# Performance work log

Measured on AMD Instinct MI355X. Metric: run time of the kernel, lower is better.

The kernel has to match this reference:

```python
import jax, jax.numpy as jnp
import numpy as np

E, P, H, V = 512, 640, 512, 1024

def setup_inputs() -> dict:
    key = jax.random.key(0)
    ks = jax.random.split(key, 8)
    s = lambda d: 1.0 / np.sqrt(d)
    return {
        "encoder_output": jax.random.normal(ks[0], (4, 256, E), jnp.float32),
        "prediction_output": jax.random.normal(ks[1], (4, 64, P), jnp.float32),
        "W_enc": jax.random.uniform(ks[2], (E, H), jnp.float32, -s(E), s(E)),
        "b_enc": jax.random.uniform(ks[3], (H,), jnp.float32, -s(E), s(E)),
        "W_pred": jax.random.uniform(ks[4], (P, H), jnp.float32, -s(P), s(P)),
        "b_pred": jax.random.uniform(ks[5], (H,), jnp.float32, -s(P), s(P)),
        "W_out": jax.random.uniform(ks[6], (H, V), jnp.float32, -s(H), s(H)),
        "b_out": jax.random.uniform(ks[7], (V,), jnp.float32, -s(H), s(H)),
    }

def reference(encoder_output, prediction_output, W_enc, b_enc, W_pred, b_pred, W_out, b_out):
    # (B,T,H) and (B,U,H) projections
    enc = jnp.einsum('bte,eh->bth', encoder_output, W_enc) + b_enc
    pred = jnp.einsum('bup,ph->buh', prediction_output, W_pred) + b_pred
    # broadcast add -> (B,T,U,H), ReLU, (dropout is identity in eval), final linear -> (B,T,U,V)
    joint = jax.nn.relu(enc[:, :, None, :] + pred[:, None, :, :])
    return jnp.einsum('btuh,hv->btuv', joint, W_out) + b_out
```

## Files before the change

### kernel.cpp

```cpp
#include <hip/hip_runtime.h>
#include <hip/hip_bf16.h>


typedef __attribute__((ext_vector_type(4))) float f32x4;
typedef __attribute__((ext_vector_type(8))) short bf16x8;

__device__ __forceinline__ short f2bf(float x) {
    return __builtin_bit_cast(short, __float2bfloat16(x));
}

__device__ __forceinline__ int swz(int r, int kByte) {
    return r * 128 + (kByte ^ ((r & 7) << 4));
}

__device__ __forceinline__ int eswz(int r, int vByte) {
    return r * 512 + (vByte ^ ((r & 7) << 4));
}

__global__ void prep_kernel(const float* __restrict__ W_enc,
                            const float* __restrict__ W_pred,
                            const float* __restrict__ W_out,
                            short* __restrict__ WencT,
                            short* __restrict__ WpredT,
                            short* __restrict__ WoutT) {
    const float* in; short* out; int R, C;
    switch (blockIdx.z) {
        case 0:  in = W_enc;  out = WencT;  R = 512; C = 512;  break;
        case 1:  in = W_pred; out = WpredT; R = 640; C = 512;  break;
        default: in = W_out;  out = WoutT;  R = 512; C = 1024; break;
    }
    const int c0 = blockIdx.x * 32, r0 = blockIdx.y * 32;
    if (c0 >= C || r0 >= R) return;

    __shared__ float tile[32][33];
    const int tx = threadIdx.x, ty = threadIdx.y;
    #pragma unroll
    for (int i = 0; i < 32; i += 8) {
        int r = r0 + ty + i, c = c0 + tx;
        if (r < R && c < C) tile[ty + i][tx] = in[(size_t)r * C + c];
    }
    __syncthreads();
    #pragma unroll
    for (int i = 0; i < 32; i += 8) {
        int oc = c0 + ty + i;
        int orr = r0 + tx;
        if (oc < C && orr < R) out[(size_t)oc * R + orr] = f2bf(tile[tx][ty + i]);
    }
}

__global__ __launch_bounds__(256, 2)
void proj_kernel(const float* __restrict__ encIn, const float* __restrict__ predIn,
                 const short* __restrict__ WencT, const short* __restrict__ WpredT,
                 const float* __restrict__ b_enc, const float* __restrict__ b_pred,
                 float* __restrict__ encA, float* __restrict__ predA) {
    const float* A; const short* BT; const float* bias; float* C;
    int M, K;
    if (blockIdx.z == 0) {
        A = encIn;  BT = WencT;  bias = b_enc;  C = encA;  M = 1024; K = 512;
    } else {
        A = predIn; BT = WpredT; bias = b_pred; C = predA; M = 256;  K = 640;
        if ((int)blockIdx.x * 128 >= M) return;
    }
    const int N = 512;

    __shared__ __align__(16) unsigned char lA[128 * 128];
    __shared__ __align__(16) unsigned char lB[128 * 128];

    const int tid = threadIdx.x;
    const int m0 = blockIdx.x * 128;
    const int n0 = blockIdx.y * 128;

    const int rSt = tid >> 3;
    const int kc  = tid & 7;

    const int wave = tid >> 6, lane = tid & 63;
    const int wr = wave >> 1, wc = wave & 1;
    const int rA0 = wr * 64 + (lane & 15);
    const int rB0 = wc * 64 + (lane & 15);
    const int kHi = (lane >> 4) * 16;

    f32x4 acc[4][4];
    #pragma unroll
    for (int i = 0; i < 4; ++i)
        #pragma unroll
        for (int j = 0; j < 4; ++j) acc[i][j] = (f32x4)0.0f;

    for (int k0 = 0; k0 < K; k0 += 64) {
        #pragma unroll
        for (int it = 0; it < 4; ++it) {
            int r = rSt + it * 32;
            const float* ap = A + (size_t)(m0 + r) * K + k0 + kc * 8;
            f32x4 a0 = *(const f32x4*)ap;
            f32x4 a1 = *(const f32x4*)(ap + 4);
            bf16x8 v;
            v[0] = f2bf(a0[0]); v[1] = f2bf(a0[1]); v[2] = f2bf(a0[2]); v[3] = f2bf(a0[3]);
            v[4] = f2bf(a1[0]); v[5] = f2bf(a1[1]); v[6] = f2bf(a1[2]); v[7] = f2bf(a1[3]);
            *(bf16x8*)(lA + swz(r, kc * 16)) = v;
        }
        #pragma unroll
        for (int it = 0; it < 4; ++it) {
            int rn = rSt + it * 32;
            const short* wp = BT + (size_t)(n0 + rn) * K + k0 + kc * 8;
            *(bf16x8*)(lB + swz(rn, kc * 16)) = *(const bf16x8*)wp;
        }
        __syncthreads();
        #pragma unroll
        for (int ks = 0; ks < 2; ++ks) {
            const int kb = ks * 64 + kHi;
            bf16x8 af[4], bf[4];
            #pragma unroll
            for (int i = 0; i < 4; ++i) af[i] = *(const bf16x8*)(lA + swz(rA0 + i * 16, kb));
            #pragma unroll
            for (int j = 0; j < 4; ++j) bf[j] = *(const bf16x8*)(lB + swz(rB0 + j * 16, kb));
            #pragma unroll
            for (int i = 0; i < 4; ++i)
                #pragma unroll
                for (int j = 0; j < 4; ++j)
                    acc[i][j] = __builtin_amdgcn_mfma_f32_16x16x32_bf16(af[i], bf[j], acc[i][j], 0, 0, 0);
        }
        __syncthreads();
    }

    #pragma unroll
    for (int i = 0; i < 4; ++i) {
        #pragma unroll
        for (int j = 0; j < 4; ++j) {
            int col = n0 + wc * 64 + j * 16 + (lane & 15);
            float bo = bias[col];
            #pragma unroll
            for (int rg = 0; rg < 4; ++rg) {
                int row = m0 + wr * 64 + i * 16 + (lane >> 4) * 4 + rg;
                C[(size_t)row * N + col] = acc[i][j][rg] + bo;
            }
        }
    }
}

__global__ __launch_bounds__(256, 2)
void joint_kernel(const float* __restrict__ encA,
                  const float* __restrict__ predA,
                  const short* __restrict__ WoutT,
                  const float* __restrict__ b_out,
                  float* __restrict__ out) {
    __shared__ __align__(16) unsigned char lA[128 * 128];
    __shared__ __align__(16) unsigned char lB[256 * 128];

    const int tid = threadIdx.x;
    const int m0 = blockIdx.x * 128;
    const int n0 = blockIdx.y * 256;
    const int b  = m0 >> 14;
    const int t0 = (m0 >> 6) & 255;

    const int rSt = tid >> 3;
    const int kc  = tid & 7;

    const int wave = tid >> 6, lane = tid & 63;
    const int wr = wave >> 1, wc = wave & 1;
    const int rA0 = wr * 64 + (lane & 15);
    const int rB0 = wc * 128 + (lane & 15);
    const int kHi = (lane >> 4) * 16;

    const float* encB  = encA + (size_t)(b * 256 + t0) * 512;
    const float* predB = predA + (size_t)(b * 64) * 512;

    f32x4 acc[4][8];
    #pragma unroll
    for (int i = 0; i < 4; ++i)
        #pragma unroll
        for (int j = 0; j < 8; ++j) acc[i][j] = (f32x4)0.0f;

    for (int k0 = 0; k0 < 512; k0 += 64) {
        #pragma unroll
        for (int it = 0; it < 4; ++it) {
            int r = rSt + it * 32;
            int tt = r >> 6;
            int u  = r & 63;
            const float* ep = encB + (size_t)tt * 512 + k0 + kc * 8;
            const float* pp = predB + (size_t)u * 512 + k0 + kc * 8;
            f32x4 e0 = *(const f32x4*)ep;
            f32x4 e1 = *(const f32x4*)(ep + 4);
            f32x4 p0 = *(const f32x4*)pp;
            f32x4 p1 = *(const f32x4*)(pp + 4);
            bf16x8 v;
            v[0] = f2bf(fmaxf(e0[0] + p0[0], 0.f));
            v[1] = f2bf(fmaxf(e0[1] + p0[1], 0.f));
            v[2] = f2bf(fmaxf(e0[2] + p0[2], 0.f));
            v[3] = f2bf(fmaxf(e0[3] + p0[3], 0.f));
            v[4] = f2bf(fmaxf(e1[0] + p1[0], 0.f));
            v[5] = f2bf(fmaxf(e1[1] + p1[1], 0.f));
            v[6] = f2bf(fmaxf(e1[2] + p1[2], 0.f));
            v[7] = f2bf(fmaxf(e1[3] + p1[3], 0.f));
            *(bf16x8*)(lA + swz(r, kc * 16)) = v;
        }
        #pragma unroll
        for (int it = 0; it < 8; ++it) {
            int rn = rSt + it * 32;
            const short* wp = WoutT + (size_t)(n0 + rn) * 512 + k0 + kc * 8;
            *(bf16x8*)(lB + swz(rn, kc * 16)) = *(const bf16x8*)wp;
        }
        __syncthreads();
        #pragma unroll
        for (int ks = 0; ks < 2; ++ks) {
            const int kb = ks * 64 + kHi;
            bf16x8 af[4], bf[8];
            #pragma unroll
            for (int i = 0; i < 4; ++i) af[i] = *(const bf16x8*)(lA + swz(rA0 + i * 16, kb));
            #pragma unroll
            for (int j = 0; j < 8; ++j) bf[j] = *(const bf16x8*)(lB + swz(rB0 + j * 16, kb));
            #pragma unroll
            for (int i = 0; i < 4; ++i)
                #pragma unroll
                for (int j = 0; j < 8; ++j)
                    acc[i][j] = __builtin_amdgcn_mfma_f32_16x16x32_bf16(af[i], bf[j], acc[i][j], 0, 0, 0);
        }
        __syncthreads();
    }

    #pragma unroll
    for (int i = 0; i < 4; ++i) {
        #pragma unroll
        for (int j = 0; j < 8; ++j) {
            int col = n0 + wc * 128 + j * 16 + (lane & 15);
            float bo = b_out[col];
            #pragma unroll
            for (int rg = 0; rg < 4; ++rg) {
                int row = m0 + wr * 64 + i * 16 + (lane >> 4) * 4 + rg;
                out[(size_t)row * 1024 + col] = acc[i][j][rg] + bo;
            }
        }
    }
}

extern "C" void kernel_launch(void* const* d_in, const int* in_sizes, int n_in,
                              void* d_out, int out_size, void* d_ws, size_t ws_size,
                              hipStream_t stream) {
    const float* enc_in  = (const float*)d_in[0];
    const float* pred_in = (const float*)d_in[1];
    const float* W_enc   = (const float*)d_in[2];
    const float* b_enc   = (const float*)d_in[3];
    const float* W_pred  = (const float*)d_in[4];
    const float* b_pred  = (const float*)d_in[5];
    const float* W_out   = (const float*)d_in[6];
    const float* b_out   = (const float*)d_in[7];
    float* out = (float*)d_out;

    char* ws = (char*)d_ws;
    float* encA   = (float*)(ws);
    float* predA  = (float*)(ws + 2097152);
    short* WencT  = (short*)(ws + 2621440);
    short* WpredT = (short*)(ws + 3145728);
    short* WoutT  = (short*)(ws + 3801088);

    prep_kernel<<<dim3(32, 20, 3), dim3(32, 8), 0, stream>>>(
        W_enc, W_pred, W_out, WencT, WpredT, WoutT);

    proj_kernel<<<dim3(8, 4, 2), 256, 0, stream>>>(
        enc_in, pred_in, WencT, WpredT, b_enc, b_pred, encA, predA);

    joint_kernel<<<dim3(65536 / 128, 1024 / 256), 256, 0, stream>>>(
        encA, predA, WoutT, b_out, out);
}
```

Measured before the change: 398.1 us.

## Pre-swizzle W_out into LDS tile layout and load via global_load_lds

The prep kernel now writes W_out as bf16 in per-(N-block, K-step) 32KB tiles that already carry the XOR swizzle the joint kernel expects. The joint kernel then copies each B tile straight from global memory into LDS with the direct global-to-LDS load instruction, so the data no longer passes through VGPRs and ds_write. This cuts register use and VALU/LDS-write traffic in the main loop. The cost is a prep pass with uncoalesced strided reads of W_out, plus reliance on the async LDS load finishing correctly before the barrier.

```diff
diff --git a/kernel.cpp b/kernel.cpp
--- a/kernel.cpp
+++ b/kernel.cpp
@@ -13,8 +13,10 @@
     return r * 128 + (kByte ^ ((r & 7) << 4));
 }
 
-__device__ __forceinline__ int eswz(int r, int vByte) {
-    return r * 512 + (vByte ^ ((r & 7) << 4));
+__device__ __forceinline__ void gload_lds16(const void* g, void* l) {
+    __builtin_amdgcn_global_load_lds(
+        (const __attribute__((address_space(1))) unsigned int*)g,
+        (__attribute__((address_space(3))) unsigned int*)l, 16, 0, 0);
 }
 
 __global__ void prep_kernel(const float* __restrict__ W_enc,
@@ -22,18 +24,37 @@
                             const float* __restrict__ W_out,
                             short* __restrict__ WencT,
                             short* __restrict__ WpredT,
-                            short* __restrict__ WoutT) {
+                            short* __restrict__ WoutS) {
+    __shared__ float tile[32][33];
+    const int tx = threadIdx.x, ty = threadIdx.y;
+
+    if (blockIdx.z == 2) {
+        const int ks = blockIdx.x, y = blockIdx.y;
+        if (ks >= 8 || y >= 4) return;
+        const int tid = ty * 32 + tx;
+        short* dst = WoutS + (size_t)(y * 8 + ks) * 16384;
+        #pragma unroll
+        for (int rg = 0; rg < 8; ++rg) {
+            int rn  = rg * 32 + (tid >> 3);
+            int ce8 = (tid & 7) * 8;
+            bf16x8 v;
+            #pragma unroll
+            for (int d = 0; d < 8; ++d) {
+                int ce = ce8 + d;
+                int h  = ks * 64 + (ce ^ ((rn & 7) << 3));
+                v[d] = f2bf(W_out[(size_t)h * 1024 + y * 256 + rn]);
+            }
+            *(bf16x8*)(dst + (size_t)rn * 64 + ce8) = v;
+        }
+        return;
+    }
+
     const float* in; short* out; int R, C;
-    switch (blockIdx.z) {
-        case 0:  in = W_enc;  out = WencT;  R = 512; C = 512;  break;
-        case 1:  in = W_pred; out = WpredT; R = 640; C = 512;  break;
-        default: in = W_out;  out = WoutT;  R = 512; C = 1024; break;
-    }
+    if (blockIdx.z == 0) { in = W_enc;  out = WencT;  R = 512; C = 512; }
+    else                 { in = W_pred; out = WpredT; R = 640; C = 512; }
     const int c0 = blockIdx.x * 32, r0 = blockIdx.y * 32;
     if (c0 >= C || r0 >= R) return;
 
-    __shared__ float tile[32][33];
-    const int tx = threadIdx.x, ty = threadIdx.y;
     #pragma unroll
     for (int i = 0; i < 32; i += 8) {
         int r = r0 + ty + i, c = c0 + tx;
@@ -139,7 +160,7 @@
 __global__ __launch_bounds__(256, 2)
 void joint_kernel(const float* __restrict__ encA,
                   const float* __restrict__ predA,
-                  const short* __restrict__ WoutT,
+                  const short* __restrict__ WoutS,
                   const float* __restrict__ b_out,
                   float* __restrict__ out) {
     __shared__ __align__(16) unsigned char lA[128 * 128];
@@ -162,6 +183,7 @@
 
     const float* encB  = encA + (size_t)(b * 256 + t0) * 512;
     const float* predB = predA + (size_t)(b * 64) * 512;
+    const char*  wY    = (const char*)WoutS + (size_t)blockIdx.y * 8 * 32768;
 
     f32x4 acc[4][8];
     #pragma unroll
@@ -170,6 +192,12 @@
         for (int j = 0; j < 8; ++j) acc[i][j] = (f32x4)0.0f;
 
     for (int k0 = 0; k0 < 512; k0 += 64) {
+        const char* wtile = wY + (size_t)(k0 >> 6) * 32768;
+        #pragma unroll
+        for (int it = 0; it < 8; ++it) {
+            int chunk = it * 4 + wave;
+            gload_lds16(wtile + chunk * 1024 + lane * 16, lB + chunk * 1024);
+        }
         #pragma unroll
         for (int it = 0; it < 4; ++it) {
             int r = rSt + it * 32;
@@ -192,12 +220,6 @@
             v[7] = f2bf(fmaxf(e1[3] + p1[3], 0.f));
             *(bf16x8*)(lA + swz(r, kc * 16)) = v;
         }
-        #pragma unroll
-        for (int it = 0; it < 8; ++it) {
-            int rn = rSt + it * 32;
-            const short* wp = WoutT + (size_t)(n0 + rn) * 512 + k0 + kc * 8;
-            *(bf16x8*)(lB + swz(rn, kc * 16)) = *(const bf16x8*)wp;
-        }
         __syncthreads();
         #pragma unroll
         for (int ks = 0; ks < 2; ++ks) {
@@ -249,14 +271,14 @@
     float* predA  = (float*)(ws + 2097152);
     short* WencT  = (short*)(ws + 2621440);
     short* WpredT = (short*)(ws + 3145728);
-    short* WoutT  = (short*)(ws + 3801088);
+    short* WoutS  = (short*)(ws + 3801088);
 
     prep_kernel<<<dim3(32, 20, 3), dim3(32, 8), 0, stream>>>(
-        W_enc, W_pred, W_out, WencT, WpredT, WoutT);
+        W_enc, W_pred, W_out, WencT, WpredT, WoutS);
 
     proj_kernel<<<dim3(8, 4, 2), 256, 0, stream>>>(
         enc_in, pred_in, WencT, WpredT, b_enc, b_pred, encA, predA);
 
     joint_kernel<<<dim3(65536 / 128, 1024 / 256), 256, 0, stream>>>(
-        encA, predA, WoutT, b_out, out);
-}
+        encA, predA, WoutS, b_out, out);
+}
```

Result: faster. 364.5 us (-8.4%).
